# Performance work log

Hardware: AMD Instinct MI355X
Metric: run time of the kernel (lower is better)

Reference implementation:

```python
import jax, jax.numpy as jnp
import numpy as np

N_F, N_T = 211, 390
PAD_T, PAD_F = 2 * N_T, N_F  # zero_pad = (780, 211): right pad in time, bottom pad in freq
N_FILTS = 119
COCH_RESCALE = 100.0
CLAMP_MIN = 1e-8


def setup_inputs() -> dict:
    key = jax.random.key(0)
    k1, k2, k3 = jax.random.split(key, 3)
    x = jax.random.uniform(k1, (1, 1, N_F, N_T), dtype=jnp.float32)
    Ht_real = jax.random.normal(k2, (N_FILTS, N_F + PAD_F, N_T + PAD_T), dtype=jnp.float32)
    Ht_imag = jax.random.normal(k3, (N_FILTS, N_F + PAD_F, N_T + PAD_T), dtype=jnp.float32)
    return {"x": x, "Ht_real": Ht_real, "Ht_imag": Ht_imag}


def reference(x, Ht_real, Ht_imag):
    # x: [B, 1, N_F, N_T] cochleagram
    xs = x[:, 0] * COCH_RESCALE  # squeeze channel, rescale -> [B, N_F, N_T]
    # ConstantPad2d((0, PAD_T, 0, PAD_F)): pad time on the right, freq on the bottom
    xp = jnp.pad(xs, ((0, 0), (0, PAD_F), (0, PAD_T)))  # [B, 422, 1170]
    X = jnp.fft.fft2(xp)  # full (two-sided) 2D FFT, complex64
    H = Ht_real + 1j * Ht_imag  # [F, 422, 1170]
    Y = X[:, None, :, :] * H[None]  # broadcast complex multiply -> [B, F, 422, 1170]
    y = jnp.fft.ifft2(Y)
    real = jnp.real(y[:, :, :N_F, :N_T])  # crop to [B, F, 211, 390]
    power = jnp.clip(real * real, CLAMP_MIN)  # SquareReal with clamp min
    # AdaptiveAvgPool2d((1,1)) -> mean over freq/time, keep dims
    out = jnp.mean(power, axis=(-2, -1), keepdims=True)  # [B, F, 1, 1]
    return out
```

## Files before the change

### kernel.cpp

```cpp
#include <hip/hip_runtime.h>
#include <math.h>

constexpr int NF  = 119;
constexpr int D1  = 422;
constexpr int D2  = 1170;
constexpr float SNORM    = 2.0253575e-06f;
constexpr float OUTSCALE = 1.2152144e-05f;

constexpr int OFF_W390  = 0;
constexpr int OFF_T1170 = 390;
constexpr int OFF_W512  = 1170;
constexpr int OFF_CHIRP = 1682;
constexpr int OFF_U422  = 1893;
constexpr int OFF_BF    = 2104;
constexpr int OFF_BI    = 2616;
constexpr int WMAT_F    = 6272;
constexpr int X_F2      = 57408;
constexpr long long Z_F = 1102304;
constexpr int ZSTR      = 448;
constexpr long long ZPF = 424LL * ZSTR;

__device__ inline float2 cmul(float2 a, float2 b) {
  return make_float2(fmaf(a.x, b.x, -(a.y * b.y)), fmaf(a.x, b.y, a.y * b.x));
}
__device__ inline float2 cmulc(float2 a, float2 b) {
  return make_float2(fmaf(a.x, b.x, (a.y * b.y)), fmaf(a.y, b.x, -(a.x * b.y)));
}
__device__ inline void cfma(float2& c, float2 a, float2 b) {
  c.x = fmaf(a.x, b.x, fmaf(-a.y, b.y, c.x));
  c.y = fmaf(a.x, b.y, fmaf(a.y, b.x, c.y));
}

__device__ inline void fft512_lds(float2* a, const float2* w, int lt, int inv) {
  #pragma unroll
  for (int s = 0; s < 2; ++s) {
    int i = lt + (s << 8);
    int j = (int)(__brev((unsigned)i) >> 23);
    if (j > i) { float2 t = a[i]; a[i] = a[j]; a[j] = t; }
  }
  __syncthreads();
  for (int s = 1; s <= 9; ++s) {
    int half = 1 << (s - 1);
    int pos = lt & (half - 1);
    int grp = lt >> (s - 1);
    int i = (grp << s) + pos;
    int j = i + half;
    float2 tw = w[pos << (9 - s)];
    if (inv) tw.y = -tw.y;
    float2 t = cmul(a[j], tw);
    float2 ai = a[i];
    a[j] = make_float2(ai.x - t.x, ai.y - t.y);
    a[i] = make_float2(ai.x + t.x, ai.y + t.y);
    __syncthreads();
  }
}

__device__ inline void bluestein_core(float2* buf, const float2* w512s, const float2* __restrict__ Bt, int lt) {
  __syncthreads();
  fft512_lds(buf, w512s, lt, 0);
  #pragma unroll
  for (int s = 0; s < 2; ++s) { int i = lt + (s << 8); buf[i] = cmul(buf[i], Bt[i]); }
  __syncthreads();
  fft512_lds(buf, w512s, lt, 1);
}

template <int INV>
__device__ inline void dft390x3(const float2* a0, const float2* a1, const float2* a2,
                                float2* b0, float2* b1, float2* b2,
                                const float2* w, int tid,
                                float2& X0, float2& X1, float2& X2) {
  bool act = tid < 390;
  if (act) {
    int ka = tid % 30, nb = tid / 30;
    float2 c0 = make_float2(0.f, 0.f), c1 = c0, c2 = c0;
    int idx = 0, step = 13 * ka;
    #pragma unroll 6
    for (int na = 0; na < 30; ++na) {
      float2 tw = w[idx];
      if (INV) tw.y = -tw.y;
      int src = 13 * na + nb;
      cfma(c0, a0[src], tw);
      cfma(c1, a1[src], tw);
      cfma(c2, a2[src], tw);
      idx += step; if (idx >= 390) idx -= 390;
    }
    float2 t2 = w[nb * ka];
    if (INV) t2.y = -t2.y;
    int o = ka * 13 + nb;
    b0[o] = cmul(c0, t2);
    b1[o] = cmul(c1, t2);
    b2[o] = cmul(c2, t2);
  }
  __syncthreads();
  if (act) {
    int ka = tid % 30, kb = tid / 30;
    float2 c0 = make_float2(0.f, 0.f), c1 = c0, c2 = c0;
    int idx = 0, step = 30 * kb;
    #pragma unroll
    for (int nb = 0; nb < 13; ++nb) {
      float2 tw = w[idx];
      if (INV) tw.y = -tw.y;
      int src = ka * 13 + nb;
      cfma(c0, b0[src], tw);
      cfma(c1, b1[src], tw);
      cfma(c2, b2[src], tw);
      idx += step; if (idx >= 390) idx -= 390;
    }
    X0 = c0; X1 = c1; X2 = c2;
  }
  __syncthreads();
}


__global__ __launch_bounds__(512) void k_init(float2* __restrict__ ws, float* __restrict__ out) {
  int tid = threadIdx.x;
  __shared__ float2 bufE[512], bufO[512];
  __shared__ float2 w512s[512];
  __shared__ float2 chirps[211];
  const double PI = 3.14159265358979323846;
  for (int j = tid; j < 390; j += 512) {
    double a = -2.0 * PI * (double)j / 390.0; double s, c; sincos(a, &s, &c);
    ws[OFF_W390 + j] = make_float2((float)c, (float)s);
  }
  for (int j = tid; j < 780; j += 512) {
    double a = 2.0 * PI * (double)j / 1170.0; double s, c; sincos(a, &s, &c);
    ws[OFF_T1170 + j] = make_float2((float)c, (float)s);
  }
  for (int j = tid; j < 512; j += 512) {
    double a = -2.0 * PI * (double)j / 512.0; double s, c; sincos(a, &s, &c);
    float2 v = make_float2((float)c, (float)s);
    ws[OFF_W512 + j] = v; w512s[j] = v;
  }
  for (int n = tid; n < 211; n += 512) {
    int m = (n * n) % 422;
    double a = PI * (double)m / 211.0; double s, c; sincos(a, &s, &c);
    float2 v = make_float2((float)c, (float)s);
    ws[OFF_CHIRP + n] = v; chirps[n] = v;
  }
  for (int p = tid; p < 211; p += 512) {
    double a = 2.0 * PI * (double)p / 422.0; double s, c; sincos(a, &s, &c);
    ws[OFF_U422 + p] = make_float2((float)c, (float)s);
  }
  if (tid < NF) out[tid] = 0.0f;
  __syncthreads();
  int g = tid >> 8, lt = tid & 255;
  float2* buf = g ? bufO : bufE;
  #pragma unroll
  for (int s = 0; s < 2; ++s) {
    int i = lt + (s << 8);
    float2 v = make_float2(0.f, 0.f);
    if (i < 211) v = chirps[i];
    else if (i >= 302) v = chirps[512 - i];
    buf[i] = v;
  }
  __syncthreads();
  fft512_lds(buf, w512s, lt, 0);
  const float sc = 1.0f / 512.0f;
  if (g == 0) {
    #pragma unroll
    for (int s = 0; s < 2; ++s) {
      int i = lt + (s << 8);
      float2 v = buf[i];
      v.x *= sc; v.y *= sc;
      ws[OFF_BF + i] = v;
    }
  }
}

__global__ __launch_bounds__(256) void k_initw(float* __restrict__ wsf) {
  int k = blockIdx.x;
  int p = threadIdx.x;
  int k1 = k >> 1;
  float v = 0.f;
  if (p < 211) {
    int m = (p * k1) % 422;
    double a = 2.0 * 3.14159265358979323846 * (double)m / 422.0;
    double s, c; sincos(a, &s, &c);
    float cf = (k1 == 0 || k1 == 211) ? 1.f : 2.f;
    v = ((k & 1) ? -(float)s : (float)c) * cf * SNORM;
  }
  wsf[WMAT_F + k * 256 + p] = v;
}

__global__ __launch_bounds__(448) void k_rowfft(const float* __restrict__ x, float* __restrict__ wsf) {
  int i = blockIdx.x;
  int tid = threadIdx.x;
  float2* ws = (float2*)wsf;
  __shared__ float2 a0[390], a1[390], a2[390], b0[390], b1[390], b2[390];
  __shared__ float2 w390s[390];
  __shared__ float2 t1170s[780];
  for (int j = tid; j < 390; j += 448) w390s[j] = ws[OFF_W390 + j];
  for (int j = tid; j < 780; j += 448) t1170s[j] = ws[OFF_T1170 + j];
  __syncthreads();
  for (int j = tid; j < 390; j += 448) {
    float xv = 100.0f * x[i * 390 + j];
    a0[j] = make_float2(xv, 0.0f);
    float2 t1 = t1170s[j];
    a1[j] = make_float2(xv * t1.x, -xv * t1.y);
    float2 t2 = t1170s[2 * j];
    a2[j] = make_float2(xv * t2.x, -xv * t2.y);
  }
  __syncthreads();
  float2 X0 = make_float2(0,0), X1 = X0, X2 = X0;
  dft390x3<0>(a0, a1, a2, b0, b1, b2, w390s, tid, X0, X1, X2);
  if (tid < 390) {
    float2* X = ws + X_F2;
    size_t base = (size_t)i * D2 + 3 * (size_t)tid;
    X[base + 0] = X0; X[base + 1] = X1; X[base + 2] = X2;
  }
}

__global__ __launch_bounds__(512) void k_colfft(float* __restrict__ wsf) {
  int tid = threadIdx.x;
  int q0 = blockIdx.x * 8;
  int ncols = min(8, D2 - q0);
  float2* ws = (float2*)wsf;
  __shared__ float Xre[8][212], Xim[8][212];
  __shared__ float2 bufE[512], bufO[512];
  __shared__ float2 w512s[512], chirps[211], u422s[211];
  for (int j = tid; j < 512; j += 512) w512s[j] = ws[OFF_W512 + j];
  for (int j = tid; j < 211; j += 512) { chirps[j] = ws[OFF_CHIRP + j]; u422s[j] = ws[OFF_U422 + j]; }
  float2* X = ws + X_F2;
  const float2* Bf = ws + OFF_BF;
  for (int idx = tid; idx < 211 * 8; idx += 512) {
    int i = idx >> 3, c = idx & 7;
    float2 v = make_float2(0.f, 0.f);
    if (c < ncols) v = X[(size_t)i * D2 + q0 + c];
    Xre[c][i] = v.x; Xim[c][i] = v.y;
  }
  __syncthreads();
  int g = tid >> 8, lt = tid & 255;
  float2* buf = g ? bufO : bufE;
  for (int c = 0; c < ncols; ++c) {
    #pragma unroll
    for (int s = 0; s < 2; ++s) {
      int i2 = lt + (s << 8);
      float2 v = make_float2(0.f, 0.f);
      if (i2 < 211) {
        v = make_float2(Xre[c][i2], Xim[c][i2]);
        if (g) v = cmulc(v, u422s[i2]);
        v = cmulc(v, chirps[i2]);
      }
      buf[i2] = v;
    }
    bluestein_core(buf, w512s, Bf, lt);
    #pragma unroll
    for (int s = 0; s < 2; ++s) {
      int i2 = lt + (s << 8);
      if (i2 < 211) {
        float2 r = cmulc(buf[i2], chirps[i2]);
        X[(size_t)(2 * i2 + g) * D2 + q0 + c] = r;
      }
    }
    __syncthreads();
  }
}

__global__ __launch_bounds__(448) void k_stage1(const float* __restrict__ Hr, const float* __restrict__ Hi,
                                                float* __restrict__ wsf, int f0) {
  int k1 = blockIdx.x;
  int fl = blockIdx.y;
  int f = f0 + fl;
  int tid = threadIdx.x;
  float2* ws = (float2*)wsf;
  __shared__ float2 a0[390], a1[390], a2[390], b0[390], b1[390], b2[390];
  __shared__ float2 w390s[390];
  __shared__ float2 t1170s[780];
  for (int j = tid; j < 390; j += 448) w390s[j] = ws[OFF_W390 + j];
  for (int j = tid; j < 780; j += 448) t1170s[j] = ws[OFF_T1170 + j];
  const float2* X = ws + X_F2 + (size_t)k1 * D2;
  int m1 = (422 - k1) % 422;
  size_t hb  = (size_t)f * (D1 * D2) + (size_t)k1 * D2;
  size_t hmb = (size_t)f * (D1 * D2) + (size_t)m1 * D2;
  for (int k2 = tid; k2 < D2; k2 += 448) {
    float2 xv = X[k2];
    int rk = (k2 == 0) ? 0 : (D2 - k2);
    float gr = 0.5f * (Hr[hb + k2] + Hr[hmb + rk]);
    float gi = 0.5f * (Hi[hb + k2] - Hi[hmb + rk]);
    float2 y = make_float2(fmaf(xv.x, gr, -(xv.y * gi)), fmaf(xv.x, gi, xv.y * gr));
    int r = k2 % 3, m = k2 / 3;
    (r == 0 ? a0 : (r == 1 ? a1 : a2))[m] = y;
  }
  __syncthreads();
  float2 A0 = make_float2(0,0), A1 = A0, A2 = A0;
  dft390x3<1>(a0, a1, a2, b0, b1, b2, w390s, tid, A0, A1, A2);
  if (tid < 390) {
    int q = tid;
    float2 t1 = t1170s[q], t2 = t1170s[2 * q];
    float zr = A0.x + (t1.x * A1.x - t1.y * A1.y) + (t2.x * A2.x - t2.y * A2.y);
    float zi = A0.y + (t1.x * A1.y + t1.y * A1.x) + (t2.x * A2.y + t2.y * A2.x);
    float* Z = wsf + Z_F + (size_t)fl * ZPF + (size_t)(2 * k1) * ZSTR;
    Z[q] = zr;
    Z[ZSTR + q] = zi;
  }
}

__global__ __launch_bounds__(256) void k_gemm(const float* __restrict__ wsf, float* __restrict__ out, int f0) {
  int fl = blockIdx.y;
  int f = f0 + fl;
  int mt = blockIdx.x / 7, nt = blockIdx.x % 7;
  int tid = threadIdx.x;
  int pbase = mt * 64, qbase = nt * 64;
  __shared__ float As[8][64];
  __shared__ float Bs[8][64];
  const float* A = wsf + WMAT_F;
  const float* B = wsf + Z_F + (size_t)fl * ZPF;
  int kk = tid >> 5, cc = (tid & 31) << 1;
  int ty = tid >> 4, tx = tid & 15;
  float C[4][4] = {};
  for (int k0 = 0; k0 < 424; k0 += 8) {
    float2 av = *(const float2*)(A + (size_t)(k0 + kk) * 256 + pbase + cc);
    float2 bv = *(const float2*)(B + (size_t)(k0 + kk) * ZSTR + qbase + cc);
    __syncthreads();
    *(float2*)&As[kk][cc] = av;
    *(float2*)&Bs[kk][cc] = bv;
    __syncthreads();
    #pragma unroll
    for (int kq = 0; kq < 8; ++kq) {
      float4 a4 = *(const float4*)&As[kq][ty << 2];
      float4 b4 = *(const float4*)&Bs[kq][tx << 2];
      C[0][0] = fmaf(a4.x, b4.x, C[0][0]); C[0][1] = fmaf(a4.x, b4.y, C[0][1]);
      C[0][2] = fmaf(a4.x, b4.z, C[0][2]); C[0][3] = fmaf(a4.x, b4.w, C[0][3]);
      C[1][0] = fmaf(a4.y, b4.x, C[1][0]); C[1][1] = fmaf(a4.y, b4.y, C[1][1]);
      C[1][2] = fmaf(a4.y, b4.z, C[1][2]); C[1][3] = fmaf(a4.y, b4.w, C[1][3]);
      C[2][0] = fmaf(a4.z, b4.x, C[2][0]); C[2][1] = fmaf(a4.z, b4.y, C[2][1]);
      C[2][2] = fmaf(a4.z, b4.z, C[2][2]); C[2][3] = fmaf(a4.z, b4.w, C[2][3]);
      C[3][0] = fmaf(a4.w, b4.x, C[3][0]); C[3][1] = fmaf(a4.w, b4.y, C[3][1]);
      C[3][2] = fmaf(a4.w, b4.z, C[3][2]); C[3][3] = fmaf(a4.w, b4.w, C[3][3]);
    }
  }
  float acc = 0.f;
  #pragma unroll
  for (int i = 0; i < 4; ++i) {
    int p = pbase + (ty << 2) + i;
    #pragma unroll
    for (int j = 0; j < 4; ++j) {
      int q = qbase + (tx << 2) + j;
      if (p < 211 && q < 390) acc += fmaxf(C[i][j] * C[i][j], 1e-8f);
    }
  }
  for (int off = 32; off > 0; off >>= 1) acc += __shfl_down(acc, off, 64);
  __shared__ float wred[4];
  int wid = tid >> 6, lane = tid & 63;
  if (lane == 0) wred[wid] = acc;
  __syncthreads();
  if (tid == 0) {
    float tot = wred[0] + wred[1] + wred[2] + wred[3];
    atomicAdd(&out[f], tot * OUTSCALE);
  }
}

extern "C" void kernel_launch(void* const* d_in, const int* in_sizes, int n_in,
                              void* d_out, int out_size, void* d_ws, size_t ws_size,
                              hipStream_t stream) {
  const float* x  = (const float*)d_in[0];
  const float* Hr = (const float*)d_in[1];
  const float* Hi = (const float*)d_in[2];
  float* out = (float*)d_out;
  float* wsf = (float*)d_ws;

  long long availf = (long long)(ws_size / 4) - Z_F;
  int chunk = (availf > 0) ? (int)(availf / ZPF) : 1;
  if (chunk < 1) chunk = 1;
  if (chunk > NF) chunk = NF;

  k_init<<<dim3(1), dim3(512), 0, stream>>>((float2*)d_ws, out);
  k_initw<<<dim3(424), dim3(256), 0, stream>>>(wsf);
  k_rowfft<<<dim3(211), dim3(448), 0, stream>>>(x, wsf);
  k_colfft<<<dim3(147), dim3(512), 0, stream>>>(wsf);
  for (int f0 = 0; f0 < NF; f0 += chunk) {
    int nf = NF - f0;
    if (nf > chunk) nf = chunk;
    k_stage1<<<dim3(212, nf), dim3(448), 0, stream>>>(Hr, Hi, wsf, f0);
    k_gemm<<<dim3(28, nf), dim3(256), 0, stream>>>(wsf, out, f0);
  }
}
```

Baseline: 858.7 us.

## Replace per-filter inverse row DFT with fp16 MFMA GEMMs over precomputed DFT matrices

Replaces the per-filter LDS-based 390-point inverse DFT stage with an explicit dense DFT-matrix GEMM. The spectral product is built in fp16, multiplied against a precomputed fp16 1170-point inverse DFT matrix using MFMA 16x16x32 instructions, then followed by a second fp16 MFMA GEMM for the 422-length column transform with the fused square, clamp and mean reduction. Operands are loaded with direct global-to-LDS async copies. This trades extra FLOPs (a dense DFT in place of the FFT) and fp16 precision loss, with prescaling to avoid overflow, for much higher matrix-core throughput.

```diff
diff --git a/kernel.cpp b/kernel.cpp
--- a/kernel.cpp
+++ b/kernel.cpp
@@ -4,21 +4,30 @@
 constexpr int NF  = 119;
 constexpr int D1  = 422;
 constexpr int D2  = 1170;
-constexpr float SNORM    = 2.0253575e-06f;
-constexpr float OUTSCALE = 1.2152144e-05f;
 
 constexpr int OFF_W390  = 0;
 constexpr int OFF_T1170 = 390;
-constexpr int OFF_W512  = 1170;
-constexpr int OFF_CHIRP = 1682;
-constexpr int OFF_U422  = 1893;
-constexpr int OFF_BF    = 2104;
-constexpr int OFF_BI    = 2616;
-constexpr int WMAT_F    = 6272;
-constexpr int X_F2      = 57408;
-constexpr long long Z_F = 1102304;
-constexpr int ZSTR      = 448;
-constexpr long long ZPF = 424LL * ZSTR;
+constexpr int OFF_W512  = 1560;
+constexpr int OFF_CHIRP = 2072;
+constexpr int OFF_U422  = 2283;
+constexpr int OFF_BF    = 2494;
+constexpr int OFF_T422  = 3006;
+
+constexpr int KP1 = 2368;
+constexpr int KB1 = KP1 * 2;
+constexpr int ZS2 = 784;
+constexpr int KP2 = 448;
+constexpr int KB2 = KP2 * 2;
+
+constexpr float SC_A   = 9.765625e-4f;
+constexpr double S_D   = 1024.0 / (422.0 * 1170.0);
+constexpr float TH_CL  = (float)(1e-8 / (S_D * S_D));
+constexpr float FINAL  = (float)(S_D * S_D / (211.0 * 390.0));
+
+typedef _Float16 h16;
+typedef _Float16 h16x2 __attribute__((ext_vector_type(2)));
+typedef _Float16 h16x8 __attribute__((ext_vector_type(8)));
+typedef float f32x4 __attribute__((ext_vector_type(4)));
 
 __device__ inline float2 cmul(float2 a, float2 b) {
   return make_float2(fmaf(a.x, b.x, -(a.y * b.y)), fmaf(a.x, b.y, a.y * b.x));
@@ -29,6 +38,11 @@
 __device__ inline void cfma(float2& c, float2 a, float2 b) {
   c.x = fmaf(a.x, b.x, fmaf(-a.y, b.y, c.x));
   c.y = fmaf(a.x, b.y, fmaf(a.y, b.x, c.y));
+}
+
+__device__ inline void async16(const void* g, void* l) {
+  __builtin_amdgcn_global_load_lds((const __attribute__((address_space(1))) unsigned int*)g,
+                                   (__attribute__((address_space(3))) unsigned int*)l, 16, 0, 0);
 }
 
 __device__ inline void fft512_lds(float2* a, const float2* w, int lt, int inv) {
@@ -112,7 +126,7 @@
 }
 
 
-__global__ __launch_bounds__(512) void k_init(float2* __restrict__ ws, float* __restrict__ out) {
+__global__ __launch_bounds__(512) void k_init(float2* __restrict__ tab, float* __restrict__ out) {
   int tid = threadIdx.x;
   __shared__ float2 bufE[512], bufO[512];
   __shared__ float2 w512s[512];
@@ -120,26 +134,30 @@
   const double PI = 3.14159265358979323846;
   for (int j = tid; j < 390; j += 512) {
     double a = -2.0 * PI * (double)j / 390.0; double s, c; sincos(a, &s, &c);
-    ws[OFF_W390 + j] = make_float2((float)c, (float)s);
-  }
-  for (int j = tid; j < 780; j += 512) {
+    tab[OFF_W390 + j] = make_float2((float)c, (float)s);
+  }
+  for (int j = tid; j < 1170; j += 512) {
     double a = 2.0 * PI * (double)j / 1170.0; double s, c; sincos(a, &s, &c);
-    ws[OFF_T1170 + j] = make_float2((float)c, (float)s);
+    tab[OFF_T1170 + j] = make_float2((float)c, (float)s);
+  }
+  for (int j = tid; j < 422; j += 512) {
+    double a = 2.0 * PI * (double)j / 422.0; double s, c; sincos(a, &s, &c);
+    tab[OFF_T422 + j] = make_float2((float)c, (float)s);
   }
   for (int j = tid; j < 512; j += 512) {
     double a = -2.0 * PI * (double)j / 512.0; double s, c; sincos(a, &s, &c);
     float2 v = make_float2((float)c, (float)s);
-    ws[OFF_W512 + j] = v; w512s[j] = v;
+    tab[OFF_W512 + j] = v; w512s[j] = v;
   }
   for (int n = tid; n < 211; n += 512) {
     int m = (n * n) % 422;
     double a = PI * (double)m / 211.0; double s, c; sincos(a, &s, &c);
     float2 v = make_float2((float)c, (float)s);
-    ws[OFF_CHIRP + n] = v; chirps[n] = v;
+    tab[OFF_CHIRP + n] = v; chirps[n] = v;
   }
   for (int p = tid; p < 211; p += 512) {
     double a = 2.0 * PI * (double)p / 422.0; double s, c; sincos(a, &s, &c);
-    ws[OFF_U422 + p] = make_float2((float)c, (float)s);
+    tab[OFF_U422 + p] = make_float2((float)c, (float)s);
   }
   if (tid < NF) out[tid] = 0.0f;
   __syncthreads();
@@ -162,35 +180,60 @@
       int i = lt + (s << 8);
       float2 v = buf[i];
       v.x *= sc; v.y *= sc;
-      ws[OFF_BF + i] = v;
-    }
-  }
-}
-
-__global__ __launch_bounds__(256) void k_initw(float* __restrict__ wsf) {
-  int k = blockIdx.x;
-  int p = threadIdx.x;
-  int k1 = k >> 1;
-  float v = 0.f;
-  if (p < 211) {
-    int m = (p * k1) % 422;
-    double a = 2.0 * 3.14159265358979323846 * (double)m / 422.0;
-    double s, c; sincos(a, &s, &c);
-    float cf = (k1 == 0 || k1 == 211) ? 1.f : 2.f;
-    v = ((k & 1) ? -(float)s : (float)c) * cf * SNORM;
-  }
-  wsf[WMAT_F + k * 256 + p] = v;
-}
-
-__global__ __launch_bounds__(448) void k_rowfft(const float* __restrict__ x, float* __restrict__ wsf) {
+      tab[OFF_BF + i] = v;
+    }
+  }
+}
+
+__global__ __launch_bounds__(256) void k_buildB(const float2* __restrict__ tab, h16* __restrict__ B1t) {
+  int n = blockIdx.x;
+  int q = n >> 1, c = n & 1;
+  int tid = threadIdx.x;
+  __shared__ float2 t[1170];
+  for (int j = tid; j < 1170; j += 256) t[j] = tab[OFF_T1170 + j];
+  __syncthreads();
+  h16* row = B1t + (size_t)n * KP1;
+  for (int k2 = tid; k2 < 1184; k2 += 256) {
+    h16x2 h;
+    if (k2 < 1170) {
+      unsigned m = ((unsigned)q * (unsigned)k2) % 1170u;
+      float2 e = t[m];
+      h.x = (h16)(c ? e.y : e.x);
+      h.y = (h16)(c ? e.x : -e.y);
+    } else { h.x = (h16)0.f; h.y = (h16)0.f; }
+    *(h16x2*)(row + 2 * k2) = h;
+  }
+}
+
+__global__ __launch_bounds__(256) void k_buildA2(const float2* __restrict__ tab, h16* __restrict__ A2) {
+  int p = blockIdx.x;
+  int tid = threadIdx.x;
+  __shared__ float2 t[422];
+  for (int j = tid; j < 422; j += 256) t[j] = tab[OFF_T422 + j];
+  __syncthreads();
+  h16* row = A2 + (size_t)p * KP2;
+  for (int k1 = tid; k1 < 224; k1 += 256) {
+    h16x2 h; h.x = (h16)0.f; h.y = (h16)0.f;
+    if (k1 < 212) {
+      unsigned m = ((unsigned)p * (unsigned)k1) % 422u;
+      float2 e = t[m];
+      float cf = (k1 == 0 || k1 == 211) ? 1.f : 2.f;
+      h.x = (h16)(cf * e.x);
+      h.y = (h16)(-cf * e.y);
+    }
+    *(h16x2*)(row + 2 * k1) = h;
+  }
+}
+
+__global__ __launch_bounds__(448) void k_rowfft(const float* __restrict__ x, const float2* __restrict__ tab,
+                                                float2* __restrict__ X) {
   int i = blockIdx.x;
   int tid = threadIdx.x;
-  float2* ws = (float2*)wsf;
   __shared__ float2 a0[390], a1[390], a2[390], b0[390], b1[390], b2[390];
   __shared__ float2 w390s[390];
   __shared__ float2 t1170s[780];
-  for (int j = tid; j < 390; j += 448) w390s[j] = ws[OFF_W390 + j];
-  for (int j = tid; j < 780; j += 448) t1170s[j] = ws[OFF_T1170 + j];
+  for (int j = tid; j < 390; j += 448) w390s[j] = tab[OFF_W390 + j];
+  for (int j = tid; j < 780; j += 448) t1170s[j] = tab[OFF_T1170 + j];
   __syncthreads();
   for (int j = tid; j < 390; j += 448) {
     float xv = 100.0f * x[i * 390 + j];
@@ -204,24 +247,21 @@
   float2 X0 = make_float2(0,0), X1 = X0, X2 = X0;
   dft390x3<0>(a0, a1, a2, b0, b1, b2, w390s, tid, X0, X1, X2);
   if (tid < 390) {
-    float2* X = ws + X_F2;
     size_t base = (size_t)i * D2 + 3 * (size_t)tid;
     X[base + 0] = X0; X[base + 1] = X1; X[base + 2] = X2;
   }
 }
 
-__global__ __launch_bounds__(512) void k_colfft(float* __restrict__ wsf) {
+__global__ __launch_bounds__(512) void k_colfft(const float2* __restrict__ tab, float2* __restrict__ X) {
   int tid = threadIdx.x;
   int q0 = blockIdx.x * 8;
   int ncols = min(8, D2 - q0);
-  float2* ws = (float2*)wsf;
   __shared__ float Xre[8][212], Xim[8][212];
   __shared__ float2 bufE[512], bufO[512];
   __shared__ float2 w512s[512], chirps[211], u422s[211];
-  for (int j = tid; j < 512; j += 512) w512s[j] = ws[OFF_W512 + j];
-  for (int j = tid; j < 211; j += 512) { chirps[j] = ws[OFF_CHIRP + j]; u422s[j] = ws[OFF_U422 + j]; }
-  float2* X = ws + X_F2;
-  const float2* Bf = ws + OFF_BF;
+  for (int j = tid; j < 512; j += 512) w512s[j] = tab[OFF_W512 + j];
+  for (int j = tid; j < 211; j += 512) { chirps[j] = tab[OFF_CHIRP + j]; u422s[j] = tab[OFF_U422 + j]; }
+  const float2* Bf = tab + OFF_BF;
   for (int idx = tid; idx < 211 * 8; idx += 512) {
     int i = idx >> 3, c = idx & 7;
     float2 v = make_float2(0.f, 0.f);
@@ -256,98 +296,156 @@
   }
 }
 
-__global__ __launch_bounds__(448) void k_stage1(const float* __restrict__ Hr, const float* __restrict__ Hi,
-                                                float* __restrict__ wsf, int f0) {
-  int k1 = blockIdx.x;
-  int fl = blockIdx.y;
-  int f = f0 + fl;
-  int tid = threadIdx.x;
-  float2* ws = (float2*)wsf;
-  __shared__ float2 a0[390], a1[390], a2[390], b0[390], b1[390], b2[390];
-  __shared__ float2 w390s[390];
-  __shared__ float2 t1170s[780];
-  for (int j = tid; j < 390; j += 448) w390s[j] = ws[OFF_W390 + j];
-  for (int j = tid; j < 780; j += 448) t1170s[j] = ws[OFF_T1170 + j];
-  const float2* X = ws + X_F2 + (size_t)k1 * D2;
+__global__ __launch_bounds__(256) void k_buildA(const float* __restrict__ Hr, const float* __restrict__ Hi,
+                                                const float2* __restrict__ X, h16* __restrict__ A, int f0) {
+  int k1 = blockIdx.x, fl = blockIdx.y, f = f0 + fl;
+  int tid = threadIdx.x;
   int m1 = (422 - k1) % 422;
   size_t hb  = (size_t)f * (D1 * D2) + (size_t)k1 * D2;
   size_t hmb = (size_t)f * (D1 * D2) + (size_t)m1 * D2;
-  for (int k2 = tid; k2 < D2; k2 += 448) {
-    float2 xv = X[k2];
-    int rk = (k2 == 0) ? 0 : (D2 - k2);
+  const float2* Xr = X + (size_t)k1 * D2;
+  h16* Arow = A + ((size_t)fl * 212 + k1) * KP1;
+  for (int k2 = tid; k2 < 1170; k2 += 256) {
+    int rk = k2 ? 1170 - k2 : 0;
     float gr = 0.5f * (Hr[hb + k2] + Hr[hmb + rk]);
     float gi = 0.5f * (Hi[hb + k2] - Hi[hmb + rk]);
-    float2 y = make_float2(fmaf(xv.x, gr, -(xv.y * gi)), fmaf(xv.x, gi, xv.y * gr));
-    int r = k2 % 3, m = k2 / 3;
-    (r == 0 ? a0 : (r == 1 ? a1 : a2))[m] = y;
-  }
-  __syncthreads();
-  float2 A0 = make_float2(0,0), A1 = A0, A2 = A0;
-  dft390x3<1>(a0, a1, a2, b0, b1, b2, w390s, tid, A0, A1, A2);
-  if (tid < 390) {
-    int q = tid;
-    float2 t1 = t1170s[q], t2 = t1170s[2 * q];
-    float zr = A0.x + (t1.x * A1.x - t1.y * A1.y) + (t2.x * A2.x - t2.y * A2.y);
-    float zi = A0.y + (t1.x * A1.y + t1.y * A1.x) + (t2.x * A2.y + t2.y * A2.x);
-    float* Z = wsf + Z_F + (size_t)fl * ZPF + (size_t)(2 * k1) * ZSTR;
-    Z[q] = zr;
-    Z[ZSTR + q] = zi;
-  }
-}
-
-__global__ __launch_bounds__(256) void k_gemm(const float* __restrict__ wsf, float* __restrict__ out, int f0) {
+    float2 xv = Xr[k2];
+    float yr = (xv.x * gr - xv.y * gi) * SC_A;
+    float yi = (xv.x * gi + xv.y * gr) * SC_A;
+    h16x2 h; h.x = (h16)yr; h.y = (h16)yi;
+    *(h16x2*)(Arow + 2 * k2) = h;
+  }
+  if (tid < 28) Arow[2340 + tid] = (h16)0.f;
+}
+
+__global__ __launch_bounds__(256) void k_gemm1(const h16* __restrict__ A, const h16* __restrict__ B1t,
+                                               h16* __restrict__ Z) {
   int fl = blockIdx.y;
-  int f = f0 + fl;
   int mt = blockIdx.x / 7, nt = blockIdx.x % 7;
-  int tid = threadIdx.x;
-  int pbase = mt * 64, qbase = nt * 64;
-  __shared__ float As[8][64];
-  __shared__ float Bs[8][64];
-  const float* A = wsf + WMAT_F;
-  const float* B = wsf + Z_F + (size_t)fl * ZPF;
-  int kk = tid >> 5, cc = (tid & 31) << 1;
-  int ty = tid >> 4, tx = tid & 15;
-  float C[4][4] = {};
-  for (int k0 = 0; k0 < 424; k0 += 8) {
-    float2 av = *(const float2*)(A + (size_t)(k0 + kk) * 256 + pbase + cc);
-    float2 bv = *(const float2*)(B + (size_t)(k0 + kk) * ZSTR + qbase + cc);
-    __syncthreads();
-    *(float2*)&As[kk][cc] = av;
-    *(float2*)&Bs[kk][cc] = bv;
-    __syncthreads();
-    #pragma unroll
-    for (int kq = 0; kq < 8; ++kq) {
-      float4 a4 = *(const float4*)&As[kq][ty << 2];
-      float4 b4 = *(const float4*)&Bs[kq][tx << 2];
-      C[0][0] = fmaf(a4.x, b4.x, C[0][0]); C[0][1] = fmaf(a4.x, b4.y, C[0][1]);
-      C[0][2] = fmaf(a4.x, b4.z, C[0][2]); C[0][3] = fmaf(a4.x, b4.w, C[0][3]);
-      C[1][0] = fmaf(a4.y, b4.x, C[1][0]); C[1][1] = fmaf(a4.y, b4.y, C[1][1]);
-      C[1][2] = fmaf(a4.y, b4.z, C[1][2]); C[1][3] = fmaf(a4.y, b4.w, C[1][3]);
-      C[2][0] = fmaf(a4.z, b4.x, C[2][0]); C[2][1] = fmaf(a4.z, b4.y, C[2][1]);
-      C[2][2] = fmaf(a4.z, b4.z, C[2][2]); C[2][3] = fmaf(a4.z, b4.w, C[2][3]);
-      C[3][0] = fmaf(a4.w, b4.x, C[3][0]); C[3][1] = fmaf(a4.w, b4.y, C[3][1]);
-      C[3][2] = fmaf(a4.w, b4.z, C[3][2]); C[3][3] = fmaf(a4.w, b4.w, C[3][3]);
-    }
-  }
-  float acc = 0.f;
+  const int M0 = mt ? 84 : 0;
+  const int N0 = (nt == 6) ? 652 : nt * 128;
+  int tid = threadIdx.x, wv = tid >> 6, ln = tid & 63;
+  int l15 = ln & 15, l16 = ln >> 4;
+  int wm = (wv >> 1) * 64, wn = (wv & 1) * 64;
+  __shared__ __align__(16) h16 Alds[128 * 32];
+  __shared__ __align__(16) h16 Blds[128 * 32];
+  const char* Ag = (const char*)(A + (size_t)fl * 212 * KP1);
+  const char* Bg = (const char*)B1t;
+  f32x4 acc[4][4] = {};
+  for (int kc = 0; kc < 74; ++kc) {
+    int kb = kc * 64;
+    __syncthreads();
+    #pragma unroll
+    for (int s = 0; s < 2; ++s) {
+      int L = ((wv * 2 + s) * 64 + ln) * 16;
+      int row = L >> 6, colb = L & 63;
+      async16(Ag + (size_t)(M0 + row) * KB1 + kb + colb, (char*)Alds + (wv * 2 + s) * 1024);
+      async16(Bg + (size_t)(N0 + row) * KB1 + kb + colb, (char*)Blds + (wv * 2 + s) * 1024);
+    }
+    __syncthreads();
+    h16x8 af[4], bf[4];
+    const h16x8* Av = (const h16x8*)Alds;
+    const h16x8* Bv = (const h16x8*)Blds;
+    #pragma unroll
+    for (int i = 0; i < 4; ++i) af[i] = Av[(wm + i * 16 + l15) * 4 + l16];
+    #pragma unroll
+    for (int j = 0; j < 4; ++j) bf[j] = Bv[(wn + j * 16 + l15) * 4 + l16];
+    #pragma unroll
+    for (int i = 0; i < 4; ++i)
+      #pragma unroll
+      for (int j = 0; j < 4; ++j)
+        acc[i][j] = __builtin_amdgcn_mfma_f32_16x16x32_f16(af[i], bf[j], acc[i][j], 0, 0, 0);
+  }
+  h16* Zf = Z + (size_t)fl * 212 * ZS2;
   #pragma unroll
   for (int i = 0; i < 4; ++i) {
-    int p = pbase + (ty << 2) + i;
     #pragma unroll
     for (int j = 0; j < 4; ++j) {
-      int q = qbase + (tx << 2) + j;
-      if (p < 211 && q < 390) acc += fmaxf(C[i][j] * C[i][j], 1e-8f);
-    }
-  }
-  for (int off = 32; off > 0; off >>= 1) acc += __shfl_down(acc, off, 64);
+      #pragma unroll
+      for (int r = 0; r < 4; ++r) {
+        int m = M0 + wm + i * 16 + l16 * 4 + r;
+        int n = N0 + wn + j * 16 + l15;
+        Zf[(size_t)m * ZS2 + n] = (h16)acc[i][j][r];
+      }
+    }
+  }
+}
+
+__global__ __launch_bounds__(256) void k_gemm2(const h16* __restrict__ A2, const h16* __restrict__ Z,
+                                               float* __restrict__ out, int f0) {
+  int fl = blockIdx.y, f = f0 + fl;
+  int mt = blockIdx.x / 7, nt = blockIdx.x % 7;
+  const int M0 = (mt == 3) ? 147 : mt * 64;
+  const int pmin = (mt == 3) ? 192 : 0;
+  const int N0 = (nt == 6) ? 326 : nt * 64;
+  const int qmin = (nt == 6) ? 384 : 0;
+  int tid = threadIdx.x, wv = tid >> 6, ln = tid & 63;
+  int l15 = ln & 15, l16 = ln >> 4;
+  int wm = (wv >> 1) * 32, wn = (wv & 1) * 32;
+  __shared__ __align__(16) h16 Alds[64 * 32];
+  __shared__ __align__(16) h16 Blds[64 * 32];
+  const char* Ag = (const char*)A2;
+  const h16* Zf = Z + (size_t)fl * 212 * ZS2;
+  f32x4 acc[2][2] = {};
+  int brow = tid >> 4, bseg = tid & 15;
+  for (int kc = 0; kc < 14; ++kc) {
+    __syncthreads();
+    {
+      int L = (wv * 64 + ln) * 16;
+      int row = L >> 6, colb = L & 63;
+      async16(Ag + (size_t)(M0 + row) * KB2 + kc * 64 + colb, (char*)Alds + wv * 1024);
+    }
+    {
+      int k1r = kc * 16 + brow;
+      uint2 u0 = make_uint2(0, 0), u1 = make_uint2(0, 0);
+      if (k1r < 212) {
+        const uint2* src = (const uint2*)(Zf + (size_t)k1r * ZS2 + 2 * N0 + bseg * 8);
+        u0 = src[0]; u1 = src[1];
+      }
+      unsigned int w[4] = {u0.x, u0.y, u1.x, u1.y};
+      unsigned short* Bs = (unsigned short*)Blds;
+      #pragma unroll
+      for (int h = 0; h < 4; ++h) {
+        int qh = bseg * 4 + h;
+        Bs[qh * 32 + 2 * brow + 0] = (unsigned short)(w[h] & 0xffffu);
+        Bs[qh * 32 + 2 * brow + 1] = (unsigned short)(w[h] >> 16);
+      }
+    }
+    __syncthreads();
+    h16x8 af[2], bf[2];
+    const h16x8* Av = (const h16x8*)Alds;
+    const h16x8* Bv = (const h16x8*)Blds;
+    af[0] = Av[(wm + l15) * 4 + l16];
+    af[1] = Av[(wm + 16 + l15) * 4 + l16];
+    bf[0] = Bv[(wn + l15) * 4 + l16];
+    bf[1] = Bv[(wn + 16 + l15) * 4 + l16];
+    #pragma unroll
+    for (int i = 0; i < 2; ++i)
+      #pragma unroll
+      for (int j = 0; j < 2; ++j)
+        acc[i][j] = __builtin_amdgcn_mfma_f32_16x16x32_f16(af[i], bf[j], acc[i][j], 0, 0, 0);
+  }
+  float accs = 0.f;
+  #pragma unroll
+  for (int i = 0; i < 2; ++i) {
+    #pragma unroll
+    for (int j = 0; j < 2; ++j) {
+      #pragma unroll
+      for (int r = 0; r < 4; ++r) {
+        int p = M0 + wm + i * 16 + l16 * 4 + r;
+        int q = N0 + wn + j * 16 + l15;
+        if (p >= pmin && q >= qmin) {
+          float y = acc[i][j][r];
+          accs += fmaxf(y * y, TH_CL);
+        }
+      }
+    }
+  }
+  for (int off = 32; off > 0; off >>= 1) accs += __shfl_down(accs, off, 64);
   __shared__ float wred[4];
-  int wid = tid >> 6, lane = tid & 63;
-  if (lane == 0) wred[wid] = acc;
-  __syncthreads();
-  if (tid == 0) {
-    float tot = wred[0] + wred[1] + wred[2] + wred[3];
-    atomicAdd(&out[f], tot * OUTSCALE);
-  }
+  if (ln == 0) wred[wv] = accs;
+  __syncthreads();
+  if (tid == 0) atomicAdd(&out[f], (wred[0] + wred[1] + wred[2] + wred[3]) * FINAL);
 }
 
 extern "C" void kernel_launch(void* const* d_in, const int* in_sizes, int n_in,
@@ -357,21 +455,33 @@
   const float* Hr = (const float*)d_in[1];
   const float* Hi = (const float*)d_in[2];
   float* out = (float*)d_out;
-  float* wsf = (float*)d_ws;
-
-  long long availf = (long long)(ws_size / 4) - Z_F;
-  int chunk = (availf > 0) ? (int)(availf / ZPF) : 1;
+  char* base = (char*)d_ws;
+
+  size_t off = 0;
+  auto alloc = [&](size_t bytes) { size_t cur = off; off = (off + bytes + 255) & ~(size_t)255; return cur; };
+  float2* tab = (float2*)(base + alloc(32768));
+  float2* X   = (float2*)(base + alloc((size_t)D1 * D2 * sizeof(float2)));
+  h16* B1t    = (h16*)(base + alloc((size_t)780 * KP1 * 2));
+  h16* A2     = (h16*)(base + alloc((size_t)211 * KP2 * 2));
+  size_t perA = (size_t)212 * KP1 * 2;
+  size_t perZ = (size_t)212 * ZS2 * 2;
+  long long avail = (long long)ws_size - (long long)off - 512;
+  int chunk = (avail > 0) ? (int)(avail / (long long)(perA + perZ)) : 1;
   if (chunk < 1) chunk = 1;
   if (chunk > NF) chunk = NF;
-
-  k_init<<<dim3(1), dim3(512), 0, stream>>>((float2*)d_ws, out);
-  k_initw<<<dim3(424), dim3(256), 0, stream>>>(wsf);
-  k_rowfft<<<dim3(211), dim3(448), 0, stream>>>(x, wsf);
-  k_colfft<<<dim3(147), dim3(512), 0, stream>>>(wsf);
+  h16* A = (h16*)(base + alloc(perA * chunk));
+  h16* Zp = (h16*)(base + alloc(perZ * chunk));
+
+  k_init<<<dim3(1), dim3(512), 0, stream>>>(tab, out);
+  k_buildB<<<dim3(780), dim3(256), 0, stream>>>(tab, B1t);
+  k_buildA2<<<dim3(211), dim3(256), 0, stream>>>(tab, A2);
+  k_rowfft<<<dim3(211), dim3(448), 0, stream>>>(x, tab, X);
+  k_colfft<<<dim3(147), dim3(512), 0, stream>>>(tab, X);
   for (int f0 = 0; f0 < NF; f0 += chunk) {
     int nf = NF - f0;
     if (nf > chunk) nf = chunk;
-    k_stage1<<<dim3(212, nf), dim3(448), 0, stream>>>(Hr, Hi, wsf, f0);
-    k_gemm<<<dim3(28, nf), dim3(256), 0, stream>>>(wsf, out, f0);
-  }
-}
+    k_buildA<<<dim3(212, nf), dim3(256), 0, stream>>>(Hr, Hi, X, A, f0);
+    k_gemm1<<<dim3(14, nf), dim3(256), 0, stream>>>(A, B1t, Zp);
+    k_gemm2<<<dim3(28, nf), dim3(256), 0, stream>>>(A2, Zp, out, f0);
+  }
+}
```

Measured after the change: 779.8 us. 1.1x faster.
